# Kernel tuning notes

Hardware: AMD Instinct MI355X
Metric: run time of the kernel (lower is better)

The kernel has to match this reference:

```python
import jax, jax.numpy as jnp
import numpy as np

B, S, D, H = 2, 2048, 2048, 16
HD = D // H
SCALE = 1.0 / np.sqrt(HD)


def setup_inputs() -> dict:
    key = jax.random.key(0)
    ks = jax.random.split(key, 11)
    xav = np.sqrt(6.0 / (D + D))  # xavier uniform bound for square weights
    def w(k):
        return jax.random.uniform(k, (D, D), jnp.float32, -xav, xav)
    return {
        "query": jax.random.normal(ks[0], (B, S, D), jnp.float32),
        "key": jax.random.normal(ks[1], (B, S, D), jnp.float32),
        "value": jax.random.normal(ks[2], (B, S, D), jnp.float32),
        "Wq": w(ks[3]), "bq": jnp.zeros((D,), jnp.float32),
        "Wk": w(ks[4]), "bk": jnp.zeros((D,), jnp.float32),
        "Wv": w(ks[5]), "bv": jnp.zeros((D,), jnp.float32),
        "Wo": w(ks[6]), "bo": jnp.zeros((D,), jnp.float32),
    }


def reference(query, key, value, Wq, bq, Wk, bk, Wv, bv, Wo, bo):
    # projections (torch Linear: x @ W.T + b)
    q = query @ Wq.T + bq
    k = key @ Wk.T + bk
    v = value @ Wv.T + bv
    # [B, H, S, HD]
    q = q.reshape(B, S, H, HD).transpose(0, 2, 1, 3)
    k = k.reshape(B, S, H, HD).transpose(0, 2, 1, 3)
    v = v.reshape(B, S, H, HD).transpose(0, 2, 1, 3)
    scores = jnp.einsum("bhqd,bhkd->bhqk", q, k) * SCALE
    causal = jnp.triu(jnp.ones((S, S), bool), k=1)
    scores = jnp.where(causal, -jnp.inf, scores)
    attn = jax.nn.softmax(scores, axis=-1)  # dropout p=0.0 -> identity
    out = jnp.einsum("bhqk,bhkd->bhqd", attn, v)
    out = out.transpose(0, 2, 1, 3).reshape(B, S, D)
    return out @ Wo.T + bo
```

## Files before the change

### kernel.cpp

```cpp
#include <hip/hip_runtime.h>
#include <hip/hip_bf16.h>


#define LOG2E 1.44269504088896340736f

typedef __attribute__((ext_vector_type(8))) short short8;
typedef __attribute__((ext_vector_type(4))) short short4b;
typedef __attribute__((ext_vector_type(4))) float floatx4;

__device__ __forceinline__ short f2bf(float f) {
  unsigned int u = __builtin_bit_cast(unsigned int, f);
  u += 0x7FFFu + ((u >> 16) & 1u);
  return (short)(u >> 16);
}

__device__ __forceinline__ short4b pack4bf(float a, float b, float c, float d) {
  __hip_bfloat162 lo = __float22bfloat162_rn(float2{a, b});
  __hip_bfloat162 hi = __float22bfloat162_rn(float2{c, d});
  short4b r;
  r[0] = __builtin_bit_cast(short, lo.x); r[1] = __builtin_bit_cast(short, lo.y);
  r[2] = __builtin_bit_cast(short, hi.x); r[3] = __builtin_bit_cast(short, hi.y);
  return r;
}

__device__ __forceinline__ void gl_lds16(const void* g, void* l) {
  __builtin_amdgcn_global_load_lds(
      (const __attribute__((address_space(1))) unsigned int*)g,
      (__attribute__((address_space(3))) unsigned int*)l, 16, 0, 0);
}

__global__ __launch_bounds__(256) void cvt_k(
    const float* __restrict__ s0, const float* __restrict__ s1,
    const float* __restrict__ s2, const float* __restrict__ s3,
    unsigned short* __restrict__ d0, unsigned short* __restrict__ d1,
    unsigned short* __restrict__ d2, unsigned short* __restrict__ d3, int n)
{
  const float* s; unsigned short* d;
  switch (blockIdx.y) {
    case 0: s = s0; d = d0; break;
    case 1: s = s1; d = d1; break;
    case 2: s = s2; d = d2; break;
    default: s = s3; d = d3; break;
  }
  const int i = (blockIdx.x * 256 + threadIdx.x) * 8;
  if (i >= n) return;
  float4 a = *(const float4*)(s + i);
  float4 b = *(const float4*)(s + i + 4);
  short8 v = (short8){f2bf(a.x), f2bf(a.y), f2bf(a.z), f2bf(a.w),
                      f2bf(b.x), f2bf(b.y), f2bf(b.z), f2bf(b.w)};
  *(short8*)(d + i) = v;
}

template<bool OUT_BF16, bool VT_OUT>
__global__ __launch_bounds__(512, 1) void gemm8_k(
    const unsigned short* __restrict__ A, const unsigned short* __restrict__ Bt,
    const float* __restrict__ bias, void* __restrict__ Cptr,
    int M, int N, int K, float alpha)
{
  __shared__ __align__(16) unsigned short As[3][256 * 64];
  __shared__ __align__(16) unsigned short Bs[3][128 * 64];
  (void)M;

  const int tid  = threadIdx.x;
  const int lane = tid & 63;
  const int wave = tid >> 6;
  const int quad = lane >> 4;
  const int l16  = lane & 15;
  const int lx7  = l16 & 7;
  const int wm   = wave >> 1, wn = wave & 1;

  int bx, by;
  if (gridDim.x == 16 && gridDim.y == 16) {
    const int lin  = (int)(blockIdx.y * 16 + blockIdx.x);
    const int xcd  = lin & 7;
    const int slot = lin >> 3;
    bx = (xcd & 1) * 8 + (slot & 7);
    by = (xcd >> 1) * 4 + (slot >> 3);
  } else { bx = (int)blockIdx.x; by = (int)blockIdx.y; }
  const long bm  = (long)by * 256;
  const long bn  = (long)bx * 128;

  const unsigned short* gA[4]; int lAo[4];
  const unsigned short* gB[2]; int lBo[2];
#pragma unroll
  for (int j = 0; j < 4; ++j) {
    const int pa = ((j >> 1) * 16 + wave * 2 + (j & 1)) * 64 + lane;
    const int r = pa >> 3, cp = pa & 7, cs = cp ^ (r & 7);
    gA[j]  = A + (bm + r) * (long)K + cs * 8;
    lAo[j] = pa * 8;
  }
#pragma unroll
  for (int j = 0; j < 2; ++j) {
    const int pb = (wave * 2 + j) * 64 + lane;
    const int r = pb >> 3, cp = pb & 7, cs = cp ^ (r & 7);
    gB[j]  = Bt + (bn + r) * (long)K + cs * 8;
    lBo[j] = pb * 8;
  }

  floatx4 acc[4][4];
#pragma unroll
  for (int i = 0; i < 4; ++i)
#pragma unroll
    for (int j = 0; j < 4; ++j) acc[i][j] = (floatx4){0.f, 0.f, 0.f, 0.f};

  const int NT = K >> 6;

#pragma unroll
  for (int j = 0; j < 4; ++j) gl_lds16(gA[j], &As[0][lAo[j]]);
#pragma unroll
  for (int j = 0; j < 2; ++j) gl_lds16(gB[j], &Bs[0][lBo[j]]);
  if (NT > 1) {
#pragma unroll
    for (int j = 0; j < 4; ++j) gl_lds16(gA[j] + 64, &As[1][lAo[j]]);
#pragma unroll
    for (int j = 0; j < 2; ++j) gl_lds16(gB[j] + 64, &Bs[1][lBo[j]]);
    asm volatile("s_waitcnt vmcnt(6)" ::: "memory");
  } else {
    asm volatile("s_waitcnt vmcnt(0)" ::: "memory");
  }
  __builtin_amdgcn_s_barrier();

  int cur = 0;
  for (int t = 0; t < NT; ++t) {
    int nx2 = cur + 2; if (nx2 >= 3) nx2 -= 3;
    const long kk2 = (long)(t + 2) * 64;
    const bool st  = (t + 2) < NT;
    const unsigned short* Ab = As[cur];
    const unsigned short* Bb = Bs[cur];

    short8 af[4][2];
#pragma unroll
    for (int mt = 0; mt < 4; ++mt)
#pragma unroll
      for (int ks = 0; ks < 2; ++ks)
        af[mt][ks] = *(const short8*)&Ab[(wm * 64 + mt * 16 + l16) * 64 +
                                         (((ks * 4 + quad) ^ lx7) * 8)];

    short8 bf00 = *(const short8*)&Bb[(wn * 64 +  0 + l16) * 64 + (((0 + quad) ^ lx7) * 8)];
    short8 bf01 = *(const short8*)&Bb[(wn * 64 +  0 + l16) * 64 + (((4 + quad) ^ lx7) * 8)];
    short8 bf10 = *(const short8*)&Bb[(wn * 64 + 16 + l16) * 64 + (((0 + quad) ^ lx7) * 8)];
    short8 bf11 = *(const short8*)&Bb[(wn * 64 + 16 + l16) * 64 + (((4 + quad) ^ lx7) * 8)];
    if (st) { gl_lds16(gA[0] + kk2, &As[nx2][lAo[0]]);
              gl_lds16(gA[1] + kk2, &As[nx2][lAo[1]]);
              gl_lds16(gA[2] + kk2, &As[nx2][lAo[2]]); }
    __builtin_amdgcn_s_barrier();
    asm volatile("s_waitcnt lgkmcnt(0)");
    __builtin_amdgcn_s_setprio(1);
#pragma unroll
    for (int mt = 0; mt < 4; ++mt) {
      acc[mt][0] = __builtin_amdgcn_mfma_f32_16x16x32_bf16(af[mt][0], bf00, acc[mt][0], 0, 0, 0);
      acc[mt][0] = __builtin_amdgcn_mfma_f32_16x16x32_bf16(af[mt][1], bf01, acc[mt][0], 0, 0, 0);
      acc[mt][1] = __builtin_amdgcn_mfma_f32_16x16x32_bf16(af[mt][0], bf10, acc[mt][1], 0, 0, 0);
      acc[mt][1] = __builtin_amdgcn_mfma_f32_16x16x32_bf16(af[mt][1], bf11, acc[mt][1], 0, 0, 0);
    }
    __builtin_amdgcn_s_setprio(0);
    __builtin_amdgcn_s_barrier();

    bf00 = *(const short8*)&Bb[(wn * 64 + 32 + l16) * 64 + (((0 + quad) ^ lx7) * 8)];
    bf01 = *(const short8*)&Bb[(wn * 64 + 32 + l16) * 64 + (((4 + quad) ^ lx7) * 8)];
    bf10 = *(const short8*)&Bb[(wn * 64 + 48 + l16) * 64 + (((0 + quad) ^ lx7) * 8)];
    bf11 = *(const short8*)&Bb[(wn * 64 + 48 + l16) * 64 + (((4 + quad) ^ lx7) * 8)];
    if (st) { gl_lds16(gA[3] + kk2, &As[nx2][lAo[3]]);
              gl_lds16(gB[0] + kk2, &Bs[nx2][lBo[0]]);
              gl_lds16(gB[1] + kk2, &Bs[nx2][lBo[1]]); }
    __builtin_amdgcn_s_barrier();
    asm volatile("s_waitcnt lgkmcnt(0)");
    __builtin_amdgcn_s_setprio(1);
#pragma unroll
    for (int mt = 0; mt < 4; ++mt) {
      acc[mt][2] = __builtin_amdgcn_mfma_f32_16x16x32_bf16(af[mt][0], bf00, acc[mt][2], 0, 0, 0);
      acc[mt][2] = __builtin_amdgcn_mfma_f32_16x16x32_bf16(af[mt][1], bf01, acc[mt][2], 0, 0, 0);
      acc[mt][3] = __builtin_amdgcn_mfma_f32_16x16x32_bf16(af[mt][0], bf10, acc[mt][3], 0, 0, 0);
      acc[mt][3] = __builtin_amdgcn_mfma_f32_16x16x32_bf16(af[mt][1], bf11, acc[mt][3], 0, 0, 0);
    }
    __builtin_amdgcn_s_setprio(0);
    if (t + 1 < NT) {
      if (st) asm volatile("s_waitcnt vmcnt(6)" ::: "memory");
      else    asm volatile("s_waitcnt vmcnt(0)" ::: "memory");
    }
    __builtin_amdgcn_s_barrier();

    cur = cur + 1 >= 3 ? 0 : cur + 1;
  }

  if (VT_OUT) {
    __syncthreads();
    unsigned short* Ct = &As[0][0];
#pragma unroll
    for (int nt = 0; nt < 4; ++nt) {
      const int col_l = wn * 64 + nt * 16 + l16;
      const float bval = bias[bn + col_l];
#pragma unroll
      for (int mt = 0; mt < 4; ++mt) {
        const int row_l = wm * 64 + mt * 16 + quad * 4;
#pragma unroll
        for (int rg = 0; rg < 4; ++rg)
          Ct[col_l * 264 + row_l + rg] = (unsigned short)f2bf((acc[mt][nt][rg] + bval) * alpha);
      }
    }
    __syncthreads();
    const int b  = (int)(bm >> 11);
    const int s0 = (int)(bm & 2047);
    const int d   = tid >> 2;
    const int seg = tid & 3;
    unsigned short* dst = (unsigned short*)Cptr +
        ((long)(b * 16 + bx) * 128 + d) * 2048 + s0 + seg * 64;
    const unsigned short* src = &Ct[d * 264 + seg * 64];
#pragma unroll
    for (int c = 0; c < 8; ++c)
      *(uint4*)(dst + c * 8) = *(const uint4*)(src + c * 8);
  } else {
#pragma unroll
    for (int nt = 0; nt < 4; ++nt) {
      const long col = bn + wn * 64 + nt * 16 + l16;
      const float bval = bias[col];
#pragma unroll
      for (int mt = 0; mt < 4; ++mt) {
#pragma unroll
        for (int rg = 0; rg < 4; ++rg) {
          const long row = bm + wm * 64 + mt * 16 + quad * 4 + rg;
          const float v = (acc[mt][nt][rg] + bval) * alpha;
          if (OUT_BF16) ((unsigned short*)Cptr)[row * (long)N + col] = (unsigned short)f2bf(v);
          else          ((float*)Cptr)[row * (long)N + col] = v;
        }
      }
    }
  }
}

template<bool A_BF16, bool OUT_BF16, bool VT_OUT>
__global__ __launch_bounds__(256, 2) void gemm_bias_k(
    const void* __restrict__ Aptr, const float* __restrict__ Bt,
    const float* __restrict__ bias, void* __restrict__ Cptr,
    int M, int N, int K, float alpha)
{
  __shared__ __align__(16) unsigned short smem[128 * 136];
  unsigned short* As = smem;
  unsigned short* Bs = smem + 128 * 40;

  const int tid  = threadIdx.x;
  const int lane = tid & 63;
  const int wave = tid >> 6;
  const int quad = lane >> 4;
  const int l16  = lane & 15;
  const int wr   = wave >> 1, wc = wave & 1;
  const long bm  = (long)blockIdx.y * 128;
  const long bn  = (long)blockIdx.x * 128;

  floatx4 acc[4][4];
#pragma unroll
  for (int i = 0; i < 4; ++i)
#pragma unroll
    for (int j = 0; j < 4; ++j) acc[i][j] = (floatx4){0.f, 0.f, 0.f, 0.f};

  const int srow = tid >> 2;
  const int cc   = tid & 3;

  for (int k0 = 0; k0 < K; k0 += 32) {
    __syncthreads();
#pragma unroll
    for (int r = 0; r < 2; ++r) {
      const int row = srow + r * 64;
      short8 av, bv;
      if (A_BF16) {
        av = *(const short8*)((const unsigned short*)Aptr + (bm + row) * (long)K + k0 + cc * 8);
      } else {
        const float* ap = (const float*)Aptr + (bm + row) * (long)K + k0 + cc * 8;
        float4 f0 = *(const float4*)ap;
        float4 f1 = *(const float4*)(ap + 4);
        av = (short8){f2bf(f0.x), f2bf(f0.y), f2bf(f0.z), f2bf(f0.w),
                      f2bf(f1.x), f2bf(f1.y), f2bf(f1.z), f2bf(f1.w)};
      }
      {
        const float* bp = Bt + (bn + row) * (long)K + k0 + cc * 8;
        float4 g0 = *(const float4*)bp;
        float4 g1 = *(const float4*)(bp + 4);
        bv = (short8){f2bf(g0.x), f2bf(g0.y), f2bf(g0.z), f2bf(g0.w),
                      f2bf(g1.x), f2bf(g1.y), f2bf(g1.z), f2bf(g1.w)};
      }
      *(short8*)&As[row * 40 + cc * 8] = av;
      *(short8*)&Bs[row * 40 + cc * 8] = bv;
    }
    __syncthreads();

    short8 af[4], bf[4];
#pragma unroll
    for (int t = 0; t < 4; ++t) {
      af[t] = *(const short8*)&As[(wr * 64 + t * 16 + l16) * 40 + quad * 8];
      bf[t] = *(const short8*)&Bs[(wc * 64 + t * 16 + l16) * 40 + quad * 8];
    }
#pragma unroll
    for (int mt = 0; mt < 4; ++mt)
#pragma unroll
      for (int nt = 0; nt < 4; ++nt)
        acc[mt][nt] = __builtin_amdgcn_mfma_f32_16x16x32_bf16(af[mt], bf[nt], acc[mt][nt], 0, 0, 0);
  }

  if (VT_OUT) {
    __syncthreads();
    unsigned short* Ct = smem;
#pragma unroll
    for (int nt = 0; nt < 4; ++nt) {
      const long col = bn + wc * 64 + nt * 16 + l16;
      const float bval = bias[col];
      const int col_l = wc * 64 + nt * 16 + l16;
#pragma unroll
      for (int mt = 0; mt < 4; ++mt) {
        const int row_l = wr * 64 + mt * 16 + quad * 4;
#pragma unroll
        for (int rg = 0; rg < 4; ++rg)
          Ct[col_l * 136 + row_l + rg] = (unsigned short)f2bf((acc[mt][nt][rg] + bval) * alpha);
      }
    }
    __syncthreads();
    const int b  = (int)(bm >> 11);
    const int s0 = (int)(bm & 2047);
    const int r    = tid >> 1;
    const int half = tid & 1;
    unsigned short* dst = (unsigned short*)Cptr +
        ((long)(b * 16 + blockIdx.x) * 128 + r) * 2048 + s0 + half * 64;
    const unsigned short* src = &Ct[r * 136 + half * 64];
#pragma unroll
    for (int c = 0; c < 8; ++c)
      *(uint4*)(dst + c * 8) = *(const uint4*)(src + c * 8);
  } else {
#pragma unroll
    for (int nt = 0; nt < 4; ++nt) {
      const long col = bn + wc * 64 + nt * 16 + l16;
      const float bval = bias[col];
#pragma unroll
      for (int mt = 0; mt < 4; ++mt) {
#pragma unroll
        for (int rg = 0; rg < 4; ++rg) {
          const long row = bm + wr * 64 + mt * 16 + quad * 4 + rg;
          const float v = (acc[mt][nt][rg] + bval) * alpha;
          if (OUT_BF16) ((unsigned short*)Cptr)[row * (long)N + col] = (unsigned short)f2bf(v);
          else          ((float*)Cptr)[row * (long)N + col] = v;
        }
      }
    }
  }
}

__global__ __launch_bounds__(256, 2) void flash_attn_k(
    const unsigned short* __restrict__ Q,
    const unsigned short* __restrict__ Kp,
    const unsigned short* __restrict__ Vt,
    unsigned short* __restrict__ O)
{
  constexpr int S = 2048, D = 2048, HD = 128;
  constexpr int PS = 72;

  __shared__ __align__(16) unsigned short Ks[2][64 * 128];
  __shared__ __align__(16) unsigned short Vst[2][128 * 64];
  __shared__ __align__(16) unsigned short Ps[64 * PS];

  const int tid  = threadIdx.x;
  const int lane = tid & 63;
  const int w    = tid >> 6;
  const int quad = lane >> 4;
  const int l16  = lane & 15;
  const int lx7  = l16 & 7;

  const int bx  = blockIdx.x;
  const int by  = blockIdx.y;
  const int idx = by * 2 + (bx >> 3);
  const int bh  = (bx & 7) * 4 + (idx >> 4);
  const int qsel = idx & 15;

  const long headoff = (long)(bh >> 4) * S * D + (long)(bh & 15) * HD;
  const long vtoff   = (long)bh * HD * S;

  const unsigned short* gK[4]; int oK[4];
  const unsigned short* gV[4]; int oV[4];
#pragma unroll
  for (int i = 0; i < 4; ++i) {
    const int p = (w * 4 + i) * 64 + lane;
    { const int r = p >> 4, cp = p & 15, c = cp ^ (r & 7);
      gK[i] = Kp + headoff + (long)r * D + c * 8;  oK[i] = p * 8; }
    { const int r = p >> 3, cp = p & 7, c = cp ^ (r & 7);
      gV[i] = Vt + vtoff + (long)r * S + c * 8;    oV[i] = p * 8; }
  }

#pragma unroll 1
  for (int half = 0; half < 2; ++half) {
    const int qt = half ? (31 - qsel) : qsel;
    const int qbase = qt * 64;
    const int qrow  = qbase + w * 16 + l16;
    const int qloc  = w * 16 + l16;

    short8 aq[4];
    {
      const unsigned short* qp = Q + headoff + (long)qrow * D;
#pragma unroll
      for (int ks = 0; ks < 4; ++ks)
        aq[ks] = *(const short8*)(qp + ks * 32 + quad * 8);
    }

    floatx4 o_acc[8];
#pragma unroll
    for (int t = 0; t < 8; ++t) o_acc[t] = (floatx4){0.f, 0.f, 0.f, 0.f};
    float m_i = -INFINITY, l_i = 0.f;

#pragma unroll
    for (int i = 0; i < 4; ++i) gl_lds16(gK[i], &Ks[0][oK[i]]);
#pragma unroll
    for (int i = 0; i < 4; ++i) gl_lds16(gV[i], &Vst[0][oV[i]]);

    for (int kt = 0; kt <= qt; ++kt) {
      const int cur = kt & 1;
      const int kbase = kt * 64;
      if (kt < qt) {
        const long kb = (long)(kt + 1) * 64;
        const int nb = cur ^ 1;
#pragma unroll
        for (int i = 0; i < 4; ++i) gl_lds16(gK[i] + kb * D, &Ks[nb][oK[i]]);
#pragma unroll
        for (int i = 0; i < 4; ++i) gl_lds16(gV[i] + kb, &Vst[nb][oV[i]]);
        asm volatile("s_waitcnt vmcnt(8)" ::: "memory");
      } else {
        asm volatile("s_waitcnt vmcnt(0)" ::: "memory");
      }
      __builtin_amdgcn_s_barrier();

      const unsigned short* Kb = &Ks[cur][0];
      const unsigned short* Vb = &Vst[cur][0];

      floatx4 sc[4];
#pragma unroll
      for (int nt = 0; nt < 4; ++nt) sc[nt] = (floatx4){0.f, 0.f, 0.f, 0.f};
      __builtin_amdgcn_s_setprio(1);
#pragma unroll
      for (int nt = 0; nt < 4; ++nt) {
        const int krow = nt * 16 + l16;
#pragma unroll
        for (int ks = 0; ks < 4; ++ks) {
          const int cp = (ks * 4 + quad) ^ lx7;
          short8 kf = *(const short8*)&Kb[krow * 128 + cp * 8];
          sc[nt] = __builtin_amdgcn_mfma_f32_16x16x32_bf16(kf, aq[ks], sc[nt], 0, 0, 0);
        }
      }
      __builtin_amdgcn_s_setprio(0);

      float sv[4][4];
      float rmax = -INFINITY;
      if (kt == qt) {
        const int kg0 = kbase + quad * 4;
#pragma unroll
        for (int nt = 0; nt < 4; ++nt)
#pragma unroll
          for (int rg = 0; rg < 4; ++rg) {
            float v = sc[nt][rg];
            if (kg0 + nt * 16 + rg > qrow) v = -INFINITY;
            sv[nt][rg] = v;
            rmax = fmaxf(rmax, v);
          }
      } else {
#pragma unroll
        for (int nt = 0; nt < 4; ++nt)
#pragma unroll
          for (int rg = 0; rg < 4; ++rg) {
            sv[nt][rg] = sc[nt][rg];
            rmax = fmaxf(rmax, sc[nt][rg]);
          }
      }
      rmax = fmaxf(rmax, __shfl_xor(rmax, 16));
      rmax = fmaxf(rmax, __shfl_xor(rmax, 32));

      float al = 1.0f;
      if (__any(rmax > m_i + 8.0f)) {
        const float mn = fmaxf(m_i, rmax);
        al = exp2f(m_i - mn);
        m_i = mn;
#pragma unroll
        for (int t = 0; t < 8; ++t)
#pragma unroll
          for (int rg = 0; rg < 4; ++rg) o_acc[t][rg] *= al;
      }

      float rsum = 0.f;
#pragma unroll
      for (int nt = 0; nt < 4; ++nt) {
        float p0 = exp2f(sv[nt][0] - m_i), p1 = exp2f(sv[nt][1] - m_i);
        float p2 = exp2f(sv[nt][2] - m_i), p3 = exp2f(sv[nt][3] - m_i);
        rsum += (p0 + p1) + (p2 + p3);
        *(short4b*)&Ps[qloc * PS + nt * 16 + quad * 4] = pack4bf(p0, p1, p2, p3);
      }
      rsum += __shfl_xor(rsum, 16);
      rsum += __shfl_xor(rsum, 32);
      l_i = l_i * al + rsum;

      short8 pf[2];
#pragma unroll
      for (int ks = 0; ks < 2; ++ks)
        pf[ks] = *(const short8*)&Ps[qloc * PS + ks * 32 + quad * 8];

      __builtin_amdgcn_s_setprio(1);
#pragma unroll
      for (int t = 0; t < 8; ++t) {
        const int drow = t * 16 + l16;
#pragma unroll
        for (int ks = 0; ks < 2; ++ks) {
          const int cp = (ks * 4 + quad) ^ lx7;
          short8 vf = *(const short8*)&Vb[drow * 64 + cp * 8];
          o_acc[t] = __builtin_amdgcn_mfma_f32_16x16x32_bf16(vf, pf[ks], o_acc[t], 0, 0, 0);
        }
      }
      __builtin_amdgcn_s_setprio(0);
      __builtin_amdgcn_s_barrier();
    }

    const float rl = 1.0f / l_i;
    unsigned short* op = O + headoff + (long)qrow * D;
#pragma unroll
    for (int t = 0; t < 8; ++t) {
      *(short4b*)(op + t * 16 + quad * 4) =
          pack4bf(o_acc[t][0] * rl, o_acc[t][1] * rl, o_acc[t][2] * rl, o_acc[t][3] * rl);
    }
  }
}

extern "C" void kernel_launch(void* const* d_in, const int* in_sizes, int n_in,
                              void* d_out, int out_size, void* d_ws, size_t ws_size,
                              hipStream_t stream) {
  const float* query = (const float*)d_in[0];
  const float* key_  = (const float*)d_in[1];
  const float* value = (const float*)d_in[2];
  const float* Wq = (const float*)d_in[3];
  const float* bq = (const float*)d_in[4];
  const float* Wk = (const float*)d_in[5];
  const float* bk = (const float*)d_in[6];
  const float* Wv = (const float*)d_in[7];
  const float* bv = (const float*)d_in[8];
  const float* Wo = (const float*)d_in[9];
  const float* bo = (const float*)d_in[10];
  float* out = (float*)d_out;

  constexpr int Bz = 2, S = 2048, D = 2048;
  constexpr int M = Bz * S;
  constexpr long NELEM = (long)M * D;
  constexpr long WELEM = (long)D * D;

  const float qscale = 0.08838834764831845f * LOG2E;
  dim3 gridG(D / 128, M / 128);
  dim3 gridG8(D / 128, M / 256);

  const size_t need_full = (size_t)(6 * NELEM + 4 * WELEM) * 2;

  if (ws_size >= need_full) {
    unsigned short* Qp  = (unsigned short*)d_ws;
    unsigned short* Kp  = Qp + NELEM;
    unsigned short* Vt  = Kp + NELEM;
    unsigned short* Xq  = Vt + NELEM;
    unsigned short* Xk  = Xq + NELEM;
    unsigned short* Xv  = Xk + NELEM;
    unsigned short* Wqb = Xv + NELEM;
    unsigned short* Wkb = Wqb + WELEM;
    unsigned short* Wvb = Wkb + WELEM;
    unsigned short* Wob = Wvb + WELEM;
    unsigned short* Oa  = Xq;

    cvt_k<<<dim3(NELEM / (8 * 256), 3), 256, 0, stream>>>(
        query, key_, value, value, Xq, Xk, Xv, Xv, (int)NELEM);
    cvt_k<<<dim3(WELEM / (8 * 256), 4), 256, 0, stream>>>(
        Wq, Wk, Wv, Wo, Wqb, Wkb, Wvb, Wob, (int)WELEM);

    gemm8_k<true, false><<<gridG8, 512, 0, stream>>>(Xq, Wqb, bq, Qp, M, D, D, qscale);
    gemm8_k<true, false><<<gridG8, 512, 0, stream>>>(Xk, Wkb, bk, Kp, M, D, D, 1.0f);
    gemm8_k<true, true ><<<gridG8, 512, 0, stream>>>(Xv, Wvb, bv, Vt, M, D, D, 1.0f);

    flash_attn_k<<<dim3(16, 32), 256, 0, stream>>>(Qp, Kp, Vt, Oa);

    gemm8_k<false, false><<<gridG8, 512, 0, stream>>>(Oa, Wob, bo, out, M, D, D, 1.0f);
  } else {
    unsigned short* Qp = (unsigned short*)d_ws;
    unsigned short* Kp = Qp + NELEM;
    unsigned short* Vt = Kp + NELEM;
    unsigned short* Oa = Vt + NELEM;

    gemm_bias_k<false, true, false><<<gridG, 256, 0, stream>>>(query, Wq, bq, Qp, M, D, D, qscale);
    gemm_bias_k<false, true, false><<<gridG, 256, 0, stream>>>(key_,  Wk, bk, Kp, M, D, D, 1.0f);
    gemm_bias_k<false, true, true ><<<gridG, 256, 0, stream>>>(value, Wv, bv, Vt, M, D, D, 1.0f);

    flash_attn_k<<<dim3(16, 32), 256, 0, stream>>>(Qp, Kp, Vt, Oa);

    gemm_bias_k<true, false, false><<<gridG, 256, 0, stream>>>(Oa, Wo, bo, out, M, D, D, 1.0f);
  }
}
```

Measured before the change: 424.8 us.

## Fuse fp32-to-bf16 activation conversion into projection GEMM A-tile loads

The separate cvt_k pass over query/key/value is removed. The projection GEMMs now read fp32 A directly through registers, convert to bf16 and write the swizzled tile into a double-buffered LDS slot, while B keeps its triple-buffered async loads. This drops one full read and write of three activation tensors, but the A path becomes a synchronous register-staged prefetch with conversion ALU work inside the main loop and double the global bytes per A tile. Separately, the flash attention kernel delays the cross-lane max reduction until a rescale is needed and defers the row-sum shuffle reduction to the end.

```diff
diff --git a/kernel.cpp b/kernel.cpp
--- a/kernel.cpp
+++ b/kernel.cpp
@@ -51,9 +51,9 @@
   *(short8*)(d + i) = v;
 }
 
-template<bool OUT_BF16, bool VT_OUT>
+template<bool A_FP32, bool OUT_BF16, bool VT_OUT>
 __global__ __launch_bounds__(512, 1) void gemm8_k(
-    const unsigned short* __restrict__ A, const unsigned short* __restrict__ Bt,
+    const void* __restrict__ Aptr, const unsigned short* __restrict__ Bt,
     const float* __restrict__ bias, void* __restrict__ Cptr,
     int M, int N, int K, float alpha)
 {
@@ -80,15 +80,7 @@
   const long bm  = (long)by * 256;
   const long bn  = (long)bx * 128;
 
-  const unsigned short* gA[4]; int lAo[4];
   const unsigned short* gB[2]; int lBo[2];
-#pragma unroll
-  for (int j = 0; j < 4; ++j) {
-    const int pa = ((j >> 1) * 16 + wave * 2 + (j & 1)) * 64 + lane;
-    const int r = pa >> 3, cp = pa & 7, cs = cp ^ (r & 7);
-    gA[j]  = A + (bm + r) * (long)K + cs * 8;
-    lAo[j] = pa * 8;
-  }
 #pragma unroll
   for (int j = 0; j < 2; ++j) {
     const int pb = (wave * 2 + j) * 64 + lane;
@@ -97,6 +89,20 @@
     lBo[j] = pb * 8;
   }
 
+  const unsigned short* gA[4]; int lAo[4];
+  const float* Af = (const float*)Aptr;
+  const int ar = tid >> 1;
+  const int ah = tid & 1;
+  if (!A_FP32) {
+#pragma unroll
+    for (int j = 0; j < 4; ++j) {
+      const int pa = ((j >> 1) * 16 + wave * 2 + (j & 1)) * 64 + lane;
+      const int r = pa >> 3, cp = pa & 7, cs = cp ^ (r & 7);
+      gA[j]  = (const unsigned short*)Aptr + (bm + r) * (long)K + cs * 8;
+      lAo[j] = pa * 8;
+    }
+  }
+
   floatx4 acc[4][4];
 #pragma unroll
   for (int i = 0; i < 4; ++i)
@@ -104,29 +110,54 @@
     for (int j = 0; j < 4; ++j) acc[i][j] = (floatx4){0.f, 0.f, 0.f, 0.f};
 
   const int NT = K >> 6;
-
-#pragma unroll
-  for (int j = 0; j < 4; ++j) gl_lds16(gA[j], &As[0][lAo[j]]);
-#pragma unroll
-  for (int j = 0; j < 2; ++j) gl_lds16(gB[j], &Bs[0][lBo[j]]);
-  if (NT > 1) {
-#pragma unroll
-    for (int j = 0; j < 4; ++j) gl_lds16(gA[j] + 64, &As[1][lAo[j]]);
-#pragma unroll
-    for (int j = 0; j < 2; ++j) gl_lds16(gB[j] + 64, &Bs[1][lBo[j]]);
-    asm volatile("s_waitcnt vmcnt(6)" ::: "memory");
+  float4 areg[8];
+
+  if (A_FP32) {
+    const float* ap0 = Af + (bm + ar) * (long)K + ah * 32;
+#pragma unroll
+    for (int j = 0; j < 8; ++j) areg[j] = *(const float4*)(ap0 + j * 4);
+#pragma unroll
+    for (int j = 0; j < 2; ++j) gl_lds16(gB[j], &Bs[0][lBo[j]]);
+    if (NT > 1) {
+#pragma unroll
+      for (int j = 0; j < 2; ++j) gl_lds16(gB[j] + 64, &Bs[1][lBo[j]]);
+    }
+#pragma unroll
+    for (int c2 = 0; c2 < 4; ++c2) {
+      const int c = ah * 4 + c2;
+      const float4 f0 = areg[2 * c2], f1 = areg[2 * c2 + 1];
+      short8 v = (short8){f2bf(f0.x), f2bf(f0.y), f2bf(f0.z), f2bf(f0.w),
+                          f2bf(f1.x), f2bf(f1.y), f2bf(f1.z), f2bf(f1.w)};
+      *(short8*)&As[0][(ar * 8 + (c ^ (ar & 7))) * 8] = v;
+    }
+    asm volatile("s_waitcnt lgkmcnt(0)" ::: "memory");
+    if (NT > 1) asm volatile("s_waitcnt vmcnt(2)" ::: "memory");
+    else        asm volatile("s_waitcnt vmcnt(0)" ::: "memory");
   } else {
-    asm volatile("s_waitcnt vmcnt(0)" ::: "memory");
+#pragma unroll
+    for (int j = 0; j < 4; ++j) gl_lds16(gA[j], &As[0][lAo[j]]);
+#pragma unroll
+    for (int j = 0; j < 2; ++j) gl_lds16(gB[j], &Bs[0][lBo[j]]);
+    if (NT > 1) {
+#pragma unroll
+      for (int j = 0; j < 4; ++j) gl_lds16(gA[j] + 64, &As[1][lAo[j]]);
+#pragma unroll
+      for (int j = 0; j < 2; ++j) gl_lds16(gB[j] + 64, &Bs[1][lBo[j]]);
+      asm volatile("s_waitcnt vmcnt(6)" ::: "memory");
+    } else {
+      asm volatile("s_waitcnt vmcnt(0)" ::: "memory");
+    }
   }
   __builtin_amdgcn_s_barrier();
 
-  int cur = 0;
+  int cur3 = 0;
   for (int t = 0; t < NT; ++t) {
-    int nx2 = cur + 2; if (nx2 >= 3) nx2 -= 3;
+    int nx2 = cur3 + 2; if (nx2 >= 3) nx2 -= 3;
     const long kk2 = (long)(t + 2) * 64;
-    const bool st  = (t + 2) < NT;
-    const unsigned short* Ab = As[cur];
-    const unsigned short* Bb = Bs[cur];
+    const bool st2 = (t + 2) < NT;
+    const bool st1 = (t + 1) < NT;
+    const unsigned short* Ab = A_FP32 ? As[t & 1] : As[cur3];
+    const unsigned short* Bb = Bs[cur3];
 
     short8 af[4][2];
 #pragma unroll
@@ -140,9 +171,17 @@
     short8 bf01 = *(const short8*)&Bb[(wn * 64 +  0 + l16) * 64 + (((4 + quad) ^ lx7) * 8)];
     short8 bf10 = *(const short8*)&Bb[(wn * 64 + 16 + l16) * 64 + (((0 + quad) ^ lx7) * 8)];
     short8 bf11 = *(const short8*)&Bb[(wn * 64 + 16 + l16) * 64 + (((4 + quad) ^ lx7) * 8)];
-    if (st) { gl_lds16(gA[0] + kk2, &As[nx2][lAo[0]]);
-              gl_lds16(gA[1] + kk2, &As[nx2][lAo[1]]);
-              gl_lds16(gA[2] + kk2, &As[nx2][lAo[2]]); }
+    if (A_FP32) {
+      if (st1) {
+        const float* ap = Af + (bm + ar) * (long)K + (long)(t + 1) * 64 + ah * 32;
+#pragma unroll
+        for (int j = 0; j < 8; ++j) areg[j] = *(const float4*)(ap + j * 4);
+      }
+    } else {
+      if (st2) { gl_lds16(gA[0] + kk2, &As[nx2][lAo[0]]);
+                 gl_lds16(gA[1] + kk2, &As[nx2][lAo[1]]);
+                 gl_lds16(gA[2] + kk2, &As[nx2][lAo[2]]); }
+    }
     __builtin_amdgcn_s_barrier();
     asm volatile("s_waitcnt lgkmcnt(0)");
     __builtin_amdgcn_s_setprio(1);
@@ -160,9 +199,11 @@
     bf01 = *(const short8*)&Bb[(wn * 64 + 32 + l16) * 64 + (((4 + quad) ^ lx7) * 8)];
     bf10 = *(const short8*)&Bb[(wn * 64 + 48 + l16) * 64 + (((0 + quad) ^ lx7) * 8)];
     bf11 = *(const short8*)&Bb[(wn * 64 + 48 + l16) * 64 + (((4 + quad) ^ lx7) * 8)];
-    if (st) { gl_lds16(gA[3] + kk2, &As[nx2][lAo[3]]);
-              gl_lds16(gB[0] + kk2, &Bs[nx2][lBo[0]]);
-              gl_lds16(gB[1] + kk2, &Bs[nx2][lBo[1]]); }
+    if (st2) {
+      if (!A_FP32) gl_lds16(gA[3] + kk2, &As[nx2][lAo[3]]);
+      gl_lds16(gB[0] + kk2, &Bs[nx2][lBo[0]]);
+      gl_lds16(gB[1] + kk2, &Bs[nx2][lBo[1]]);
+    }
     __builtin_amdgcn_s_barrier();
     asm volatile("s_waitcnt lgkmcnt(0)");
     __builtin_amdgcn_s_setprio(1);
@@ -174,13 +215,33 @@
       acc[mt][3] = __builtin_amdgcn_mfma_f32_16x16x32_bf16(af[mt][1], bf11, acc[mt][3], 0, 0, 0);
     }
     __builtin_amdgcn_s_setprio(0);
-    if (t + 1 < NT) {
-      if (st) asm volatile("s_waitcnt vmcnt(6)" ::: "memory");
-      else    asm volatile("s_waitcnt vmcnt(0)" ::: "memory");
+
+    if (A_FP32) {
+      if (st1) {
+        unsigned short* dstbuf = As[(t + 1) & 1];
+#pragma unroll
+        for (int c2 = 0; c2 < 4; ++c2) {
+          const int c = ah * 4 + c2;
+          const float4 f0 = areg[2 * c2], f1 = areg[2 * c2 + 1];
+          short8 v = (short8){f2bf(f0.x), f2bf(f0.y), f2bf(f0.z), f2bf(f0.w),
+                              f2bf(f1.x), f2bf(f1.y), f2bf(f1.z), f2bf(f1.w)};
+          *(short8*)&dstbuf[(ar * 8 + (c ^ (ar & 7))) * 8] = v;
+        }
+        asm volatile("s_waitcnt lgkmcnt(0)" ::: "memory");
+        if (st2) asm volatile("s_waitcnt vmcnt(2)" ::: "memory");
+        else     asm volatile("s_waitcnt vmcnt(0)" ::: "memory");
+      } else {
+        asm volatile("s_waitcnt vmcnt(0)" ::: "memory");
+      }
+    } else {
+      if (st1) {
+        if (st2) asm volatile("s_waitcnt vmcnt(6)" ::: "memory");
+        else     asm volatile("s_waitcnt vmcnt(0)" ::: "memory");
+      }
     }
     __builtin_amdgcn_s_barrier();
 
-    cur = cur + 1 >= 3 ? 0 : cur + 1;
+    cur3 = cur3 + 1 >= 3 ? 0 : cur3 + 1;
   }
 
   if (VT_OUT) {
@@ -400,7 +461,8 @@
     floatx4 o_acc[8];
 #pragma unroll
     for (int t = 0; t < 8; ++t) o_acc[t] = (floatx4){0.f, 0.f, 0.f, 0.f};
-    float m_i = -INFINITY, l_i = 0.f;
+    float m_i = -INFINITY;
+    float l_p = 0.f;
 
 #pragma unroll
     for (int i = 0; i < 4; ++i) gl_lds16(gK[i], &Ks[0][oK[i]]);
@@ -443,7 +505,7 @@
       __builtin_amdgcn_s_setprio(0);
 
       float sv[4][4];
-      float rmax = -INFINITY;
+      float lmax = -INFINITY;
       if (kt == qt) {
         const int kg0 = kbase + quad * 4;
 #pragma unroll
@@ -453,7 +515,7 @@
             float v = sc[nt][rg];
             if (kg0 + nt * 16 + rg > qrow) v = -INFINITY;
             sv[nt][rg] = v;
-            rmax = fmaxf(rmax, v);
+            lmax = fmaxf(lmax, v);
           }
       } else {
 #pragma unroll
@@ -461,14 +523,14 @@
 #pragma unroll
           for (int rg = 0; rg < 4; ++rg) {
             sv[nt][rg] = sc[nt][rg];
-            rmax = fmaxf(rmax, sc[nt][rg]);
+            lmax = fmaxf(lmax, sc[nt][rg]);
           }
       }
-      rmax = fmaxf(rmax, __shfl_xor(rmax, 16));
-      rmax = fmaxf(rmax, __shfl_xor(rmax, 32));
 
       float al = 1.0f;
-      if (__any(rmax > m_i + 8.0f)) {
+      if (__any(lmax > m_i + 8.0f)) {
+        float rmax = fmaxf(lmax, __shfl_xor(lmax, 16));
+        rmax = fmaxf(rmax, __shfl_xor(rmax, 32));
         const float mn = fmaxf(m_i, rmax);
         al = exp2f(m_i - mn);
         m_i = mn;
@@ -486,9 +548,7 @@
         rsum += (p0 + p1) + (p2 + p3);
         *(short4b*)&Ps[qloc * PS + nt * 16 + quad * 4] = pack4bf(p0, p1, p2, p3);
       }
-      rsum += __shfl_xor(rsum, 16);
-      rsum += __shfl_xor(rsum, 32);
-      l_i = l_i * al + rsum;
+      l_p = l_p * al + rsum;
 
       short8 pf[2];
 #pragma unroll
@@ -510,6 +570,8 @@
       __builtin_amdgcn_s_barrier();
     }
 
+    float l_i = l_p + __shfl_xor(l_p, 16);
+    l_i += __shfl_xor(l_i, 32);
     const float rl = 1.0f / l_i;
     unsigned short* op = O + headoff + (long)qrow * D;
 #pragma unroll
@@ -545,33 +607,28 @@
   dim3 gridG(D / 128, M / 128);
   dim3 gridG8(D / 128, M / 256);
 
-  const size_t need_full = (size_t)(6 * NELEM + 4 * WELEM) * 2;
+  const size_t need_full = (size_t)(4 * NELEM + 4 * WELEM) * 2;
 
   if (ws_size >= need_full) {
     unsigned short* Qp  = (unsigned short*)d_ws;
     unsigned short* Kp  = Qp + NELEM;
     unsigned short* Vt  = Kp + NELEM;
-    unsigned short* Xq  = Vt + NELEM;
-    unsigned short* Xk  = Xq + NELEM;
-    unsigned short* Xv  = Xk + NELEM;
-    unsigned short* Wqb = Xv + NELEM;
+    unsigned short* Oa  = Vt + NELEM;
+    unsigned short* Wqb = Oa + NELEM;
     unsigned short* Wkb = Wqb + WELEM;
     unsigned short* Wvb = Wkb + WELEM;
     unsigned short* Wob = Wvb + WELEM;
-    unsigned short* Oa  = Xq;
-
-    cvt_k<<<dim3(NELEM / (8 * 256), 3), 256, 0, stream>>>(
-        query, key_, value, value, Xq, Xk, Xv, Xv, (int)NELEM);
+
     cvt_k<<<dim3(WELEM / (8 * 256), 4), 256, 0, stream>>>(
         Wq, Wk, Wv, Wo, Wqb, Wkb, Wvb, Wob, (int)WELEM);
 
-    gemm8_k<true, false><<<gridG8, 512, 0, stream>>>(Xq, Wqb, bq, Qp, M, D, D, qscale);
-    gemm8_k<true, false><<<gridG8, 512, 0, stream>>>(Xk, Wkb, bk, Kp, M, D, D, 1.0f);
-    gemm8_k<true, true ><<<gridG8, 512, 0, stream>>>(Xv, Wvb, bv, Vt, M, D, D, 1.0f);
+    gemm8_k<true, true, false><<<gridG8, 512, 0, stream>>>(query, Wqb, bq, Qp, M, D, D, qscale);
+    gemm8_k<true, true, false><<<gridG8, 512, 0, stream>>>(key_,  Wkb, bk, Kp, M, D, D, 1.0f);
+    gemm8_k<true, true, true ><<<gridG8, 512, 0, stream>>>(value, Wvb, bv, Vt, M, D, D, 1.0f);
 
     flash_attn_k<<<dim3(16, 32), 256, 0, stream>>>(Qp, Kp, Vt, Oa);
 
-    gemm8_k<false, false><<<gridG8, 512, 0, stream>>>(Oa, Wob, bo, out, M, D, D, 1.0f);
+    gemm8_k<false, false, false><<<gridG8, 512, 0, stream>>>(Oa, Wob, bo, out, M, D, D, 1.0f);
   } else {
     unsigned short* Qp = (unsigned short*)d_ws;
     unsigned short* Kp = Qp + NELEM;
```

Result: slower. 631.4 us (+48.6%).
